# Optimization experiments

Hardware: AMD Instinct MI355X
Metric: run time of the kernel (lower is better)

Reference implementation:

```python
import jax, jax.numpy as jnp
import numpy as np

N, K, C = 200000, 27, 64


def setup_inputs() -> dict:
    key = jax.random.key(0)
    k1, k2, k3, k4 = jax.random.split(key, 4)
    data = jax.random.normal(k1, (N, C), dtype=jnp.float32)
    # Xavier-like scale for depthwise weights (kdim, 1, C)
    weights = jax.random.normal(k2, (K, 1, C), dtype=jnp.float32) * 0.1
    neigh = jax.random.randint(k3, (N, K), 0, N, dtype=jnp.int32)
    invalid = jax.random.uniform(k4, (N, K)) < 0.05
    neigh = jnp.where(invalid, -1, neigh)
    return {"data": data, "weights": weights, "neigh": neigh}


def reference(data, weights, neigh):
    # buffer[i,k,c] = data[neigh[i,k], c] if neigh[i,k] >= 0 else 0
    valid = neigh >= 0                                   # [N, K]
    gathered = jnp.where(valid[:, :, None],
                         data[jnp.clip(neigh, 0)],       # [N, K, C]
                         jnp.zeros((), dtype=data.dtype))
    w = weights.reshape(K, C)                            # flatten(0,1)
    out = jnp.einsum('ikc,kc->ic', gathered, w)          # depthwise conv
    return out
```

## Files before the change

kernel.cpp:

```cpp
#include <hip/hip_runtime.h>
#include <stdint.h>


typedef float    v4f __attribute__((ext_vector_type(4)));
typedef uint32_t v4u __attribute__((ext_vector_type(4)));

constexpr int K   = 27;
constexpr int C   = 64;
constexpr int RPB = 64;
constexpr int OST = 17;

__global__ __launch_bounds__(256) void absmax_kernel(
    const v4f* __restrict__ in, int* __restrict__ amax_i, int n4)
{
    __shared__ float red[256];
    float m = 0.f;
    for (int i = blockIdx.x * 256 + threadIdx.x; i < n4; i += gridDim.x * 256) {
        v4f a = __builtin_nontemporal_load(in + i);
        m = fmaxf(m, fmaxf(fmaxf(fabsf(a.x), fabsf(a.y)),
                           fmaxf(fabsf(a.z), fabsf(a.w))));
    }
    red[threadIdx.x] = m;
    __syncthreads();
    for (int s = 128; s > 0; s >>= 1) {
        if (threadIdx.x < s) red[threadIdx.x] = fmaxf(red[threadIdx.x], red[threadIdx.x + s]);
        __syncthreads();
    }
    if (threadIdx.x == 0)
        atomicMax(amax_i, __float_as_int(red[0]));
}

__device__ inline uint32_t q4(v4f x, float sq) {
    int b0 = (int)rintf(x.x * sq);
    int b1 = (int)rintf(x.y * sq);
    int b2 = (int)rintf(x.z * sq);
    int b3 = (int)rintf(x.w * sq);
    return (uint32_t)(b0 & 0xFF) | ((uint32_t)(b1 & 0xFF) << 8) |
           ((uint32_t)(b2 & 0xFF) << 16) | ((uint32_t)(b3 & 0xFF) << 24);
}

__global__ __launch_bounds__(256) void convert_kernel(
    const v4f* __restrict__ in, v4u* __restrict__ outq,
    const int* __restrict__ amax_i, int n16)
{
    const int i = blockIdx.x * 256 + threadIdx.x;
    if (i >= n16) return;
    const float amax = __int_as_float(*amax_i);
    const float sq   = 127.0f / amax;
    v4f a = __builtin_nontemporal_load(in + 4 * i);
    v4f b = __builtin_nontemporal_load(in + 4 * i + 1);
    v4f c = __builtin_nontemporal_load(in + 4 * i + 2);
    v4f d = __builtin_nontemporal_load(in + 4 * i + 3);
    v4u q;
    q.x = q4(a, sq); q.y = q4(b, sq); q.z = q4(c, sq); q.w = q4(d, sq);
    outq[i] = q;
}

__global__ __launch_bounds__(256) void gather_kernel(
    const v4u*   __restrict__ dataq,
    const float* __restrict__ weights,
    const int*   __restrict__ neigh,
    const int*   __restrict__ amax_i,
    v4f*         __restrict__ out4,
    int nrows)
{
    __shared__ float w_lds[K * C];
    __shared__ int   n_lds[RPB * K];
    __shared__ v4f   o_lds[RPB * OST];

    const int tid = threadIdx.x;
    for (int idx = tid; idx < K * C / 4; idx += 256)
        ((v4f*)w_lds)[idx] = ((const v4f*)weights)[idx];

    const long nbase = (long)blockIdx.x * RPB * K;
    const long ntot  = (long)nrows * K;
    for (int idx = tid; idx < RPB * K; idx += 256) {
        const long g = nbase + idx;
        n_lds[idx] = (g < ntot) ? __builtin_nontemporal_load(neigh + g) : -1;
    }
    __syncthreads();

    const int l     = tid & 3;
    const int group = tid >> 2;
    const int row   = blockIdx.x * RPB + group;
    if (row >= nrows) return;

    const int* __restrict__ nrow = n_lds + group * K;

    v4f acc0 = (v4f)0.f, acc1 = (v4f)0.f, acc2 = (v4f)0.f, acc3 = (v4f)0.f;

    #pragma unroll
    for (int b = 0; b < K; b += 9) {
        int nk[9];
        v4u d[9];
        #pragma unroll
        for (int j = 0; j < 9; ++j) nk[j] = nrow[b + j];
        #pragma unroll
        for (int j = 0; j < 9; ++j) {
            const int n = nk[j];
            d[j] = dataq[(n < 0 ? 0 : n) * 4 + l];
        }
        __builtin_amdgcn_sched_barrier(0);
        #pragma unroll
        for (int j = 0; j < 9; ++j) {
            if (nk[j] < 0) d[j] = (v4u){0u, 0u, 0u, 0u};
            const v4f* wv = (const v4f*)(w_lds + (b + j) * C + l * 16);
            uint32_t u;
            u = d[j].x;
            acc0 += (v4f){(float)(int8_t)(u), (float)(int8_t)(u >> 8),
                          (float)(int8_t)(u >> 16), (float)(int8_t)(u >> 24)} * wv[0];
            u = d[j].y;
            acc1 += (v4f){(float)(int8_t)(u), (float)(int8_t)(u >> 8),
                          (float)(int8_t)(u >> 16), (float)(int8_t)(u >> 24)} * wv[1];
            u = d[j].z;
            acc2 += (v4f){(float)(int8_t)(u), (float)(int8_t)(u >> 8),
                          (float)(int8_t)(u >> 16), (float)(int8_t)(u >> 24)} * wv[2];
            u = d[j].w;
            acc3 += (v4f){(float)(int8_t)(u), (float)(int8_t)(u >> 8),
                          (float)(int8_t)(u >> 16), (float)(int8_t)(u >> 24)} * wv[3];
        }
    }

    const float s = __int_as_float(*amax_i) * (1.0f / 127.0f);

    v4f* ol = o_lds + group * OST;
    ol[4 * l + 0] = acc0 * s;
    ol[4 * l + 1] = acc1 * s;
    ol[4 * l + 2] = acc2 * s;
    ol[4 * l + 3] = acc3 * s;
    v4f r0 = ol[0 * 4 + l];
    v4f r1 = ol[1 * 4 + l];
    v4f r2 = ol[2 * 4 + l];
    v4f r3 = ol[3 * 4 + l];
    v4f* o = out4 + row * (C / 4);
    __builtin_nontemporal_store(r0, o + 0 * 4 + l);
    __builtin_nontemporal_store(r1, o + 1 * 4 + l);
    __builtin_nontemporal_store(r2, o + 2 * 4 + l);
    __builtin_nontemporal_store(r3, o + 3 * 4 + l);
}

extern "C" void kernel_launch(void* const* d_in, const int* in_sizes, int n_in,
                              void* d_out, int out_size, void* d_ws, size_t ws_size,
                              hipStream_t stream) {
    const float* data    = (const float*)d_in[0];
    const float* weights = (const float*)d_in[1];
    const int*   neigh   = (const int*)d_in[2];
    v4f*         out4    = (v4f*)d_out;

    int* amax_i = (int*)d_ws;
    v4u* dataq  = (v4u*)((char*)d_ws + 256);

    const int nrows = in_sizes[0] / C;
    const int n4    = nrows * C / 4;
    const int n16   = nrows * C / 16;

    absmax_kernel<<<2048, 256, 0, stream>>>((const v4f*)data, amax_i, n4);
    convert_kernel<<<(n16 + 255) / 256, 256, 0, stream>>>(
        (const v4f*)data, dataq, amax_i, n16);

    const int blocks = (nrows + RPB - 1) / RPB;
    gather_kernel<<<blocks, 256, 0, stream>>>(
        dataq, weights, neigh, amax_i, out4, nrows);
}
```

Measured before the change: 222.5 us.

## Bucket-sort per-row neighbor indices by address range to improve gather locality

Each row's 27 neighbor indices are counting-sorted in LDS into coarse address buckets, packed together with their original kernel-offset index, so the int8 gathers are issued in address order. Weight lookups become indirect through the packed k, and the weight LDS rows are padded to reduce bank conflicts. This adds a serial per-row sort done by only 64 threads plus an extra barrier. Sorting within a single row of 27 random neighbors gives little cross-thread locality.

Result: slower. 236.6 us (+6.4%).

```diff
diff --git a/kernel.cpp b/kernel.cpp
--- a/kernel.cpp
+++ b/kernel.cpp
@@ -5,10 +5,13 @@
 typedef float    v4f __attribute__((ext_vector_type(4)));
 typedef uint32_t v4u __attribute__((ext_vector_type(4)));
 
-constexpr int K   = 27;
-constexpr int C   = 64;
-constexpr int RPB = 64;
-constexpr int OST = 17;
+constexpr int K     = 27;
+constexpr int C     = 64;
+constexpr int RPB   = 64;
+constexpr int OST   = 17;
+constexpr int WST   = 68;
+constexpr int SH    = 14;
+constexpr int NBUCK = 13;
 
 __global__ __launch_bounds__(256) void absmax_kernel(
     const v4f* __restrict__ in, int* __restrict__ amax_i, int n4)
@@ -64,13 +67,17 @@
     v4f*         __restrict__ out4,
     int nrows)
 {
-    __shared__ float w_lds[K * C];
+    __shared__ float w_lds[K * WST];
     __shared__ int   n_lds[RPB * K];
+    __shared__ int   n_srt[RPB * K];
+    __shared__ int   cnt[RPB * NBUCK];
     __shared__ v4f   o_lds[RPB * OST];
 
     const int tid = threadIdx.x;
-    for (int idx = tid; idx < K * C / 4; idx += 256)
-        ((v4f*)w_lds)[idx] = ((const v4f*)weights)[idx];
+    for (int idx = tid; idx < K * (C / 4); idx += 256) {
+        const int k = idx >> 4, c4 = idx & 15;
+        *(v4f*)(w_lds + k * WST + c4 * 4) = ((const v4f*)weights)[idx];
+    }
 
     const long nbase = (long)blockIdx.x * RPB * K;
     const long ntot  = (long)nrows * K;
@@ -80,31 +87,57 @@
     }
     __syncthreads();
 
+    if (tid < RPB) {
+        int* c = cnt + tid * NBUCK;
+        #pragma unroll
+        for (int b = 0; b < NBUCK; ++b) c[b] = 0;
+        const int* src = n_lds + tid * K;
+        #pragma unroll
+        for (int j = 0; j < K; ++j) {
+            const int v = src[j];
+            c[v < 0 ? 0 : (v >> SH)]++;
+        }
+        int off = 0;
+        #pragma unroll
+        for (int b = 0; b < NBUCK; ++b) { const int t = c[b]; c[b] = off; off += t; }
+        int* dst = n_srt + tid * K;
+        #pragma unroll
+        for (int j = 0; j < K; ++j) {
+            const int v   = src[j];
+            const int sl  = v < 0 ? 0 : (v >> SH);
+            const int pos = c[sl]++;
+            dst[pos] = (v < 0) ? (int)(0x80000000u | (unsigned)j)
+                               : ((v << 5) | j);
+        }
+    }
+    __syncthreads();
+
     const int l     = tid & 3;
     const int group = tid >> 2;
     const int row   = blockIdx.x * RPB + group;
     if (row >= nrows) return;
 
-    const int* __restrict__ nrow = n_lds + group * K;
+    const int* ns = n_srt + group * K;
 
     v4f acc0 = (v4f)0.f, acc1 = (v4f)0.f, acc2 = (v4f)0.f, acc3 = (v4f)0.f;
 
     #pragma unroll
     for (int b = 0; b < K; b += 9) {
-        int nk[9];
+        int pk[9];
         v4u d[9];
         #pragma unroll
-        for (int j = 0; j < 9; ++j) nk[j] = nrow[b + j];
+        for (int j = 0; j < 9; ++j) pk[j] = ns[b + j];
         #pragma unroll
         for (int j = 0; j < 9; ++j) {
-            const int n = nk[j];
-            d[j] = dataq[(n < 0 ? 0 : n) * 4 + l];
+            const int n = (int)(((unsigned)pk[j] >> 5) & 0x3FFFFu);
+            d[j] = dataq[n * 4 + l];
         }
         __builtin_amdgcn_sched_barrier(0);
         #pragma unroll
         for (int j = 0; j < 9; ++j) {
-            if (nk[j] < 0) d[j] = (v4u){0u, 0u, 0u, 0u};
-            const v4f* wv = (const v4f*)(w_lds + (b + j) * C + l * 16);
+            if (pk[j] < 0) d[j] = (v4u){0u, 0u, 0u, 0u};
+            const int k = pk[j] & 31;
+            const v4f* wv = (const v4f*)(w_lds + k * WST + l * 16);
             uint32_t u;
             u = d[j].x;
             acc0 += (v4f){(float)(int8_t)(u), (float)(int8_t)(u >> 8),
```
